# Kernel optimization log

Hardware: AMD Instinct MI355X
Metric: run time of the kernel (lower is better)

Reference implementation:

```python
import jax, jax.numpy as jnp
import numpy as np

N_NODES = 100000
D_FEAT = 128
N_ETYPES = 3
N_EDGES = 1000000


def setup_inputs() -> dict:
    key = jax.random.key(0)
    kx, ke = jax.random.split(key)
    x = jax.random.normal(kx, (N_NODES, D_FEAT), dtype=jnp.float32)
    # edges[t, 0] = src node ids, edges[t, 1] = dst node ids for edge type t
    edges = jax.random.randint(ke, (N_ETYPES, 2, N_EDGES), 0, N_NODES, dtype=jnp.int32)
    return {"x": x, "edges": edges}


def _copy_u_mean(x, src, dst, n_nodes):
    # gather source features and segment-mean them onto destination nodes;
    # nodes with zero in-degree get 0 (matching DGL copy_u + mean semantics)
    summed = jax.ops.segment_sum(x[src], dst, num_segments=n_nodes)  # [N, D]
    count = jax.ops.segment_sum(jnp.ones_like(dst, dtype=x.dtype), dst,
                                num_segments=n_nodes)  # [N]
    return jnp.where(count[:, None] > 0, summed / jnp.maximum(count, 1)[:, None],
                     jnp.zeros((), dtype=x.dtype))


def reference(x, edges):
    # sep=True: prepend the raw features before the per-edge-type aggregations
    parts = [x]
    for t in range(N_ETYPES):  # small fixed loop over structurally distinct edge types
        parts.append(_copy_u_mean(x, edges[t, 0], edges[t, 1], x.shape[0]))
    return jnp.concatenate(parts, axis=-1)  # [N, D*(1+N_ETYPES)]
```

## Files before the change

### kernel.cpp

```cpp
#include <hip/hip_runtime.h>
#include <hip/hip_bf16.h>

#define NN 100000
#define DF 128
#define NT 3
#define NE 1000000
#define DOUT 512
#define TOTH (NT * NN)
#define NBKT2 293
#define BCAP2 11264
#define CHUNK4 1024
#define CPT 245
#define CVT4_BLOCKS (NN * DF / 4 / 256)
#define EDGE4_BLOCKS ((NT * NE / 4 + 255) / 256)
#define SCAN_CHUNK 1024
#define NB1 ((TOTH + SCAN_CHUNK - 1) / SCAN_CHUNK)
#define NXCD 8
#define SLICE_BINS (TOTH / NXCD)

typedef __attribute__((ext_vector_type(4))) float f4v;
__device__ __forceinline__ void nts_f4(float4 v, float4* p) {
    f4v t; t.x = v.x; t.y = v.y; t.z = v.z; t.w = v.w;
    __builtin_nontemporal_store(t, (f4v*)p);
}

__global__ __launch_bounds__(256) void zero_k(int* __restrict__ p, int n) {
    int i = blockIdx.x * 256 + threadIdx.x;
    if (i < n) p[i] = 0;
}

__global__ __launch_bounds__(256) void cvtpart_k(const float4* __restrict__ x4,
                                                 uint2* __restrict__ xh2,
                                                 float4* __restrict__ out4,
                                                 const int4* __restrict__ edges4,
                                                 int* __restrict__ gcur,
                                                 int2* __restrict__ append) {
    __shared__ int cntB[512];
    __shared__ int startB[512];
    __shared__ int curB[512];
    __shared__ int targB[512];
    __shared__ int s[256];
    __shared__ int2 staged[4096];

    if (blockIdx.x < CVT4_BLOCKS) {
        int i = blockIdx.x * 256 + threadIdx.x;
        float4 v = x4[i];
        __hip_bfloat162 h0 = __float22bfloat162_rn(make_float2(v.x, v.y));
        __hip_bfloat162 h1 = __float22bfloat162_rn(make_float2(v.z, v.w));
        uint2 u; u.x = *(unsigned int*)&h0; u.y = *(unsigned int*)&h1;
        xh2[i] = u;
        int n = i >> 5;
        nts_f4(v, &out4[(size_t)n * (DOUT / 4) + (i & 31)]);
        return;
    }

    const int n4row = NE / 4;
    int b = blockIdx.x - CVT4_BLOCKS;
    int t = b / CPT;
    int c = b - t * CPT;
    int base4 = c * CHUNK4;
    int n4 = n4row - base4; if (n4 > CHUNK4) n4 = CHUNK4;
    int tid = threadIdx.x;
    for (int i = tid; i < 512; i += 256) { cntB[i] = 0; curB[i] = 0; }
    __syncthreads();

    int4 sv[4], dv[4];
    bool have[4];
#pragma unroll
    for (int j = 0; j < 4; j++) {
        int i4 = tid + j * 256;
        have[j] = (i4 < n4);
        if (have[j]) {
            sv[j] = edges4[(size_t)(2 * t) * n4row + base4 + i4];
            dv[j] = edges4[(size_t)(2 * t + 1) * n4row + base4 + i4];
            int b0 = t * NN;
            atomicAdd(&cntB[(b0 + dv[j].x) >> 10], 1);
            atomicAdd(&cntB[(b0 + dv[j].y) >> 10], 1);
            atomicAdd(&cntB[(b0 + dv[j].z) >> 10], 1);
            atomicAdd(&cntB[(b0 + dv[j].w) >> 10], 1);
        }
    }
    __syncthreads();
    int e0 = cntB[2 * tid], e1 = cntB[2 * tid + 1];
    int sum2 = e0 + e1;
    s[tid] = sum2;
    __syncthreads();
    for (int off = 1; off < 256; off <<= 1) {
        int tt = (tid >= off) ? s[tid - off] : 0;
        __syncthreads();
        s[tid] += tt;
        __syncthreads();
    }
    int run = s[tid] - sum2;
    startB[2 * tid] = run;
    startB[2 * tid + 1] = run + e0;
    __syncthreads();
#pragma unroll
    for (int j = 0; j < 4; j++) {
        if (have[j]) {
            int b0 = t * NN;
            int bin, bb, p;
            bin = b0 + dv[j].x; bb = bin >> 10; p = startB[bb] + atomicAdd(&curB[bb], 1); staged[p] = make_int2(sv[j].x, bin);
            bin = b0 + dv[j].y; bb = bin >> 10; p = startB[bb] + atomicAdd(&curB[bb], 1); staged[p] = make_int2(sv[j].y, bin);
            bin = b0 + dv[j].z; bb = bin >> 10; p = startB[bb] + atomicAdd(&curB[bb], 1); staged[p] = make_int2(sv[j].z, bin);
            bin = b0 + dv[j].w; bb = bin >> 10; p = startB[bb] + atomicAdd(&curB[bb], 1); staged[p] = make_int2(sv[j].w, bin);
        }
    }
    __syncthreads();
    for (int i = tid; i < NBKT2; i += 256)
        if (cntB[i] > 0) targB[i] = atomicAdd(&gcur[i], cntB[i]);
    __syncthreads();
    int total = n4 * 4;
    for (int i = tid; i < total; i += 256) {
        int2 e = staged[i];
        int bb = e.y >> 10;
        int gpos = targB[bb] + (i - startB[bb]);
        if (gpos < BCAP2) append[(size_t)bb * BCAP2 + gpos] = e;
    }
}

__global__ __launch_bounds__(512) void scanB_k(const int* __restrict__ gcur,
                                               int* __restrict__ bucketStart) {
    __shared__ int s[512];
    int tid = threadIdx.x;
    int v = 0;
    if (tid < NBKT2) { v = gcur[tid]; if (v > BCAP2) v = BCAP2; }
    s[tid] = v;
    __syncthreads();
    for (int off = 1; off < 512; off <<= 1) {
        int tt = (tid >= off) ? s[tid - off] : 0;
        __syncthreads();
        s[tid] += tt;
        __syncthreads();
    }
    if (tid < NBKT2) bucketStart[tid] = s[tid] - v;
}

__global__ __launch_bounds__(256) void binz_k(const int* __restrict__ gcur,
                                              const int* __restrict__ bucketStart,
                                              const int2* __restrict__ append,
                                              int* __restrict__ srcS,
                                              int2* __restrict__ cntoffs) {
    __shared__ int lcnt[1024], lofs[1024], lcur[1024];
    __shared__ int s[256];
    int bkt = blockIdx.x;
    int tid = threadIdx.x;
    int nb = gcur[bkt]; if (nb > BCAP2) nb = BCAP2;
    for (int i = tid; i < 1024; i += 256) { lcnt[i] = 0; lcur[i] = 0; }
    __syncthreads();
    const int2* ap = append + (size_t)bkt * BCAP2;
    for (int i = tid; i < nb; i += 256) atomicAdd(&lcnt[ap[i].y & 1023], 1);
    __syncthreads();
    int b4 = tid * 4;
    int v0 = lcnt[b4], v1 = lcnt[b4 + 1], v2 = lcnt[b4 + 2], v3 = lcnt[b4 + 3];
    int sum = v0 + v1 + v2 + v3;
    s[tid] = sum;
    __syncthreads();
    for (int off = 1; off < 256; off <<= 1) {
        int tt = (tid >= off) ? s[tid - off] : 0;
        __syncthreads();
        s[tid] += tt;
        __syncthreads();
    }
    int run = s[tid] - sum;
    lofs[b4] = run; run += v0;
    lofs[b4 + 1] = run; run += v1;
    lofs[b4 + 2] = run; run += v2;
    lofs[b4 + 3] = run;
    __syncthreads();
    int gbase = bucketStart[bkt];
    int binBase = bkt << 10;
    for (int i = tid; i < 1024 && binBase + i < TOTH; i += 256)
        cntoffs[binBase + i] = make_int2(lcnt[i], gbase + lofs[i]);
    for (int i = tid; i < nb; i += 256) {
        int2 e = ap[i];
        int lb = e.y & 1023;
        int pos = lofs[lb] + atomicAdd(&lcur[lb], 1);
        srcS[gbase + pos] = e.x;
    }
}

__global__ __launch_bounds__(256) void gather_agg_k(const uint2* __restrict__ xh2,
                                                    const int2* __restrict__ cntoffs,
                                                    const int* __restrict__ srcS,
                                                    float4* __restrict__ out4) {
    int gtid = blockIdx.x * 256 + threadIdx.x;
    int a = gtid >> 6;
    if (a >= TOTH) return;
    int lane = threadIdx.x & 63;
    int half = lane >> 5;
    int col = lane & 31;
    int t = a / NN;
    int n = a - t * NN;
    int2 co = cntoffs[a];
    int c = co.x;
    int base = co.y;
    float4 acc = make_float4(0.f, 0.f, 0.f, 0.f);
    int k = half;
    for (; k + 6 < c; k += 8) {
        int s0 = srcS[base + k];
        int s1 = srcS[base + k + 2];
        int s2 = srcS[base + k + 4];
        int s3 = srcS[base + k + 6];
        uint2 u0 = xh2[(size_t)s0 * 32 + col];
        uint2 u1 = xh2[(size_t)s1 * 32 + col];
        uint2 u2 = xh2[(size_t)s2 * 32 + col];
        uint2 u3 = xh2[(size_t)s3 * 32 + col];
        float2 p;
        p = __bfloat1622float2(*(__hip_bfloat162*)&u0.x); acc.x += p.x; acc.y += p.y;
        p = __bfloat1622float2(*(__hip_bfloat162*)&u0.y); acc.z += p.x; acc.w += p.y;
        p = __bfloat1622float2(*(__hip_bfloat162*)&u1.x); acc.x += p.x; acc.y += p.y;
        p = __bfloat1622float2(*(__hip_bfloat162*)&u1.y); acc.z += p.x; acc.w += p.y;
        p = __bfloat1622float2(*(__hip_bfloat162*)&u2.x); acc.x += p.x; acc.y += p.y;
        p = __bfloat1622float2(*(__hip_bfloat162*)&u2.y); acc.z += p.x; acc.w += p.y;
        p = __bfloat1622float2(*(__hip_bfloat162*)&u3.x); acc.x += p.x; acc.y += p.y;
        p = __bfloat1622float2(*(__hip_bfloat162*)&u3.y); acc.z += p.x; acc.w += p.y;
    }
    for (; k < c; k += 2) {
        int s0 = srcS[base + k];
        uint2 u0 = xh2[(size_t)s0 * 32 + col];
        float2 p;
        p = __bfloat1622float2(*(__hip_bfloat162*)&u0.x); acc.x += p.x; acc.y += p.y;
        p = __bfloat1622float2(*(__hip_bfloat162*)&u0.y); acc.z += p.x; acc.w += p.y;
    }
    acc.x += __shfl_xor(acc.x, 32, 64);
    acc.y += __shfl_xor(acc.y, 32, 64);
    acc.z += __shfl_xor(acc.z, 32, 64);
    acc.w += __shfl_xor(acc.w, 32, 64);
    if (half == 0) {
        float sc = (c > 0) ? 1.0f / (float)c : 0.0f;
        acc.x *= sc; acc.y *= sc; acc.z *= sc; acc.w *= sc;
        nts_f4(acc, &out4[(size_t)n * (DOUT / 4) + (DF / 4) + t * (DF / 4) + col]);
    }
}


__global__ __launch_bounds__(256) void hist_k(const int4* __restrict__ edges4,
                                              int* __restrict__ hist) {
    int i = blockIdx.x * 256 + threadIdx.x;
    if (i >= NT * NE / 4) return;
    int t = i / (NE / 4);
    int e4 = i - t * (NE / 4);
    int4 d = edges4[(size_t)(2 * t + 1) * (NE / 4) + e4];
    atomicAdd(&hist[t * NN + d.x], 1);
    atomicAdd(&hist[t * NN + d.y], 1);
    atomicAdd(&hist[t * NN + d.z], 1);
    atomicAdd(&hist[t * NN + d.w], 1);
}

__global__ __launch_bounds__(256) void scan1_k(const int* __restrict__ hist,
                                               int* __restrict__ offs,
                                               int* __restrict__ bsum) {
    __shared__ int s[256];
    int tid = threadIdx.x;
    int base = blockIdx.x * SCAN_CHUNK + tid * 4;
    int v0 = 0, v1 = 0, v2 = 0, v3 = 0;
    if (base + 0 < TOTH) v0 = hist[base + 0];
    if (base + 1 < TOTH) v1 = hist[base + 1];
    if (base + 2 < TOTH) v2 = hist[base + 2];
    if (base + 3 < TOTH) v3 = hist[base + 3];
    int sum = v0 + v1 + v2 + v3;
    s[tid] = sum;
    __syncthreads();
    for (int off = 1; off < 256; off <<= 1) {
        int t = (tid >= off) ? s[tid - off] : 0;
        __syncthreads();
        s[tid] += t;
        __syncthreads();
    }
    int run = s[tid] - sum;
    if (tid == 255) bsum[blockIdx.x] = s[255];
    if (base + 0 < TOTH) { offs[base + 0] = run; run += v0; }
    if (base + 1 < TOTH) { offs[base + 1] = run; run += v1; }
    if (base + 2 < TOTH) { offs[base + 2] = run; run += v2; }
    if (base + 3 < TOTH) { offs[base + 3] = run; run += v3; }
}

__global__ __launch_bounds__(512) void scan2_k(int* __restrict__ bsum) {
    __shared__ int s[512];
    int tid = threadIdx.x;
    int v = (tid < NB1) ? bsum[tid] : 0;
    s[tid] = v;
    __syncthreads();
    for (int off = 1; off < 512; off <<= 1) {
        int t = (tid >= off) ? s[tid - off] : 0;
        __syncthreads();
        s[tid] += t;
        __syncthreads();
    }
    if (tid < NB1) bsum[tid] = s[tid] - v;
}

__global__ __launch_bounds__(256) void scan3_k(int* __restrict__ offs,
                                               const int* __restrict__ bsum) {
    int i = blockIdx.x * 256 + threadIdx.x;
    if (i < TOTH) offs[i] += bsum[i / SCAN_CHUNK];
}

__global__ __launch_bounds__(256) void fill_csr_k(const int4* __restrict__ edges4,
                                                  int* __restrict__ offs,
                                                  int* __restrict__ srcS) {
    int slice = blockIdx.x & (NXCD - 1);
    int i = (blockIdx.x >> 3) * 256 + threadIdx.x;
    if (i >= NT * NE / 4) return;
    int t = i / (NE / 4);
    int e4 = i - t * (NE / 4);
    int4 sv = edges4[(size_t)(2 * t) * (NE / 4) + e4];
    int4 dv = edges4[(size_t)(2 * t + 1) * (NE / 4) + e4];
    int b0 = t * NN;
    int bin;
    bin = b0 + dv.x; if (bin / SLICE_BINS == slice) srcS[atomicAdd(&offs[bin], 1)] = sv.x;
    bin = b0 + dv.y; if (bin / SLICE_BINS == slice) srcS[atomicAdd(&offs[bin], 1)] = sv.y;
    bin = b0 + dv.z; if (bin / SLICE_BINS == slice) srcS[atomicAdd(&offs[bin], 1)] = sv.z;
    bin = b0 + dv.w; if (bin / SLICE_BINS == slice) srcS[atomicAdd(&offs[bin], 1)] = sv.w;
}

__global__ __launch_bounds__(256) void gather_f32_k(const float4* __restrict__ x4,
                                                    const int* __restrict__ cnt,
                                                    const int* __restrict__ offs,
                                                    const int* __restrict__ srcS,
                                                    float4* __restrict__ out4) {
    int gtid = blockIdx.x * 256 + threadIdx.x;
    int w = gtid >> 6;
    int lane = threadIdx.x & 63;
    int half = lane >> 5;
    int col = lane & 31;
    if (w < NN / 2) {
        int n = 2 * w + half;
        out4[(size_t)n * (DOUT / 4) + col] = x4[(size_t)n * (DF / 4) + col];
        return;
    }
    int a = w - NN / 2;
    if (a >= TOTH) return;
    int t = a / NN;
    int n = a - t * NN;
    int c = cnt[a];
    int base = offs[a] - c;
    float4 acc = make_float4(0.f, 0.f, 0.f, 0.f);
    for (int k = half; k < c; k += 2) {
        int s0 = srcS[base + k];
        float4 v0 = x4[(size_t)s0 * (DF / 4) + col];
        acc.x += v0.x; acc.y += v0.y; acc.z += v0.z; acc.w += v0.w;
    }
    acc.x += __shfl_xor(acc.x, 32, 64);
    acc.y += __shfl_xor(acc.y, 32, 64);
    acc.z += __shfl_xor(acc.z, 32, 64);
    acc.w += __shfl_xor(acc.w, 32, 64);
    if (half == 0) {
        float sc = (c > 0) ? 1.0f / (float)c : 0.0f;
        acc.x *= sc; acc.y *= sc; acc.z *= sc; acc.w *= sc;
        out4[(size_t)n * (DOUT / 4) + (DF / 4) + t * (DF / 4) + col] = acc;
    }
}

extern "C" void kernel_launch(void* const* d_in, const int* in_sizes, int n_in,
                              void* d_out, int out_size, void* d_ws, size_t ws_size,
                              hipStream_t stream) {
    const float* x = (const float*)d_in[0];
    const int* edges = (const int*)d_in[1];
    float4* out4 = (float4*)d_out;

    const int covBlocks = (TOTH + 255) / 256;
    const int aggBlocks = (TOTH * 64 + 255) / 256;

    size_t appendInts = (size_t)NBKT2 * BCAP2 * 2;
    size_t fastInts = 1024 + appendInts + 2 * (size_t)TOTH +
                      (size_t)NN * DF / 2 + (size_t)NT * NE + 64;
    if (ws_size >= fastInts * 4) {
        int* gcur = (int*)d_ws;
        int* bucketStart = gcur + 512;
        int2* append = (int2*)(bucketStart + 512);
        int2* cntoffs = (int2*)((int*)d_ws + 1024 + appendInts);
        unsigned int* xh = (unsigned int*)(cntoffs + TOTH);
        int* srcS = (int*)(xh + (size_t)NN * DF / 2);

        hipLaunchKernelGGL(zero_k, dim3(2), dim3(256), 0, stream, gcur, 512);
        hipLaunchKernelGGL(cvtpart_k, dim3(CVT4_BLOCKS + NT * CPT), dim3(256), 0,
                           stream, (const float4*)x, (uint2*)xh, (float4*)d_out,
                           (const int4*)edges, gcur, append);
        hipLaunchKernelGGL(scanB_k, dim3(1), dim3(512), 0, stream, gcur, bucketStart);
        hipLaunchKernelGGL(binz_k, dim3(NBKT2), dim3(256), 0, stream,
                           gcur, bucketStart, append, srcS, cntoffs);
        hipLaunchKernelGGL(gather_agg_k, dim3(aggBlocks), dim3(256), 0, stream,
                           (const uint2*)xh, cntoffs, srcS, out4);
        return;
    }

    int* hist = (int*)d_ws;
    int* offs = hist + TOTH;
    int* bsum = offs + TOTH;
    int* srcS = bsum + 1024;
    const int nWaves = NN / 2 + TOTH;
    const int gatherBlocks = (nWaves + 3) / 4;
    hipLaunchKernelGGL(zero_k, dim3(covBlocks), dim3(256), 0, stream, hist, TOTH);
    hipLaunchKernelGGL(hist_k, dim3(EDGE4_BLOCKS), dim3(256), 0, stream,
                       (const int4*)edges, hist);
    hipLaunchKernelGGL(scan1_k, dim3(NB1), dim3(256), 0, stream, hist, offs, bsum);
    hipLaunchKernelGGL(scan2_k, dim3(1), dim3(512), 0, stream, bsum);
    hipLaunchKernelGGL(scan3_k, dim3(covBlocks), dim3(256), 0, stream, offs, bsum);
    hipLaunchKernelGGL(fill_csr_k, dim3(EDGE4_BLOCKS * NXCD), dim3(256), 0, stream,
                       (const int4*)edges, offs, srcS);
    hipLaunchKernelGGL(gather_f32_k, dim3(gatherBlocks), dim3(256), 0, stream,
                       (const float4*)x, hist, offs, srcS, out4);
}
```

Baseline: 218.6 us.

## Fold bucket scan into binz kernel, reorder partition blocks first, widen binz

Removes the separate single-block scanB kernel launch: each binz block now redundantly computes the 293-bucket prefix sum in shared memory to get its global base. binz blocks grow from 256 to 1024 threads so each handles one bin per thread and strides the bucket edges by 1024. The fused convert/partition kernel now schedules partition blocks ahead of conversion blocks, so the slower edge-partition work starts first. The costs are redundant scan work per block and more synchronisation in larger blocks.

Measured after the change: 211.1 us. 3.4% less time.

```diff
diff --git a/kernel.cpp b/kernel.cpp
--- a/kernel.cpp
+++ b/kernel.cpp
@@ -11,6 +11,7 @@
 #define BCAP2 11264
 #define CHUNK4 1024
 #define CPT 245
+#define PART_BLOCKS (NT * CPT)
 #define CVT4_BLOCKS (NN * DF / 4 / 256)
 #define EDGE4_BLOCKS ((NT * NE / 4 + 255) / 256)
 #define SCAN_CHUNK 1024
@@ -42,8 +43,8 @@
     __shared__ int s[256];
     __shared__ int2 staged[4096];
 
-    if (blockIdx.x < CVT4_BLOCKS) {
-        int i = blockIdx.x * 256 + threadIdx.x;
+    if (blockIdx.x >= PART_BLOCKS) {
+        int i = (blockIdx.x - PART_BLOCKS) * 256 + threadIdx.x;
         float4 v = x4[i];
         __hip_bfloat162 h0 = __float22bfloat162_rn(make_float2(v.x, v.y));
         __hip_bfloat162 h1 = __float22bfloat162_rn(make_float2(v.z, v.w));
@@ -55,7 +56,7 @@
     }
 
     const int n4row = NE / 4;
-    int b = blockIdx.x - CVT4_BLOCKS;
+    int b = blockIdx.x;
     int t = b / CPT;
     int c = b - t * CPT;
     int base4 = c * CHUNK4;
@@ -119,60 +120,62 @@
     }
 }
 
-__global__ __launch_bounds__(512) void scanB_k(const int* __restrict__ gcur,
-                                               int* __restrict__ bucketStart) {
-    __shared__ int s[512];
-    int tid = threadIdx.x;
-    int v = 0;
-    if (tid < NBKT2) { v = gcur[tid]; if (v > BCAP2) v = BCAP2; }
-    s[tid] = v;
-    __syncthreads();
-    for (int off = 1; off < 512; off <<= 1) {
-        int tt = (tid >= off) ? s[tid - off] : 0;
-        __syncthreads();
-        s[tid] += tt;
-        __syncthreads();
-    }
-    if (tid < NBKT2) bucketStart[tid] = s[tid] - v;
-}
-
-__global__ __launch_bounds__(256) void binz_k(const int* __restrict__ gcur,
-                                              const int* __restrict__ bucketStart,
-                                              const int2* __restrict__ append,
-                                              int* __restrict__ srcS,
-                                              int2* __restrict__ cntoffs) {
+__global__ __launch_bounds__(1024) void binz_k(const int* __restrict__ gcur,
+                                               const int2* __restrict__ append,
+                                               int* __restrict__ srcS,
+                                               int2* __restrict__ cntoffs) {
     __shared__ int lcnt[1024], lofs[1024], lcur[1024];
     __shared__ int s[256];
+    __shared__ int sB[512];
     int bkt = blockIdx.x;
     int tid = threadIdx.x;
-    int nb = gcur[bkt]; if (nb > BCAP2) nb = BCAP2;
-    for (int i = tid; i < 1024; i += 256) { lcnt[i] = 0; lcur[i] = 0; }
-    __syncthreads();
+    int nbRaw = gcur[bkt];
+    int nb = nbRaw < BCAP2 ? nbRaw : BCAP2;
+    if (tid < 512) {
+        int v = 0;
+        if (tid < NBKT2) { v = gcur[tid]; if (v > BCAP2) v = BCAP2; }
+        sB[tid] = v;
+    }
+    lcnt[tid] = 0; lcur[tid] = 0;
+    __syncthreads();
+    for (int off = 1; off < 512; off <<= 1) {
+        int tt = 0;
+        if (tid < 512 && tid >= off) tt = sB[tid - off];
+        __syncthreads();
+        if (tid < 512) sB[tid] += tt;
+        __syncthreads();
+    }
+    int gbase = (bkt == 0) ? 0 : sB[bkt - 1];
     const int2* ap = append + (size_t)bkt * BCAP2;
-    for (int i = tid; i < nb; i += 256) atomicAdd(&lcnt[ap[i].y & 1023], 1);
+    for (int i = tid; i < nb; i += 1024) atomicAdd(&lcnt[ap[i].y & 1023], 1);
     __syncthreads();
     int b4 = tid * 4;
-    int v0 = lcnt[b4], v1 = lcnt[b4 + 1], v2 = lcnt[b4 + 2], v3 = lcnt[b4 + 3];
-    int sum = v0 + v1 + v2 + v3;
-    s[tid] = sum;
+    int v0 = 0, v1 = 0, v2 = 0, v3 = 0, sum = 0;
+    if (tid < 256) {
+        v0 = lcnt[b4]; v1 = lcnt[b4 + 1]; v2 = lcnt[b4 + 2]; v3 = lcnt[b4 + 3];
+        sum = v0 + v1 + v2 + v3;
+        s[tid] = sum;
+    }
     __syncthreads();
     for (int off = 1; off < 256; off <<= 1) {
-        int tt = (tid >= off) ? s[tid - off] : 0;
-        __syncthreads();
-        s[tid] += tt;
-        __syncthreads();
-    }
-    int run = s[tid] - sum;
-    lofs[b4] = run; run += v0;
-    lofs[b4 + 1] = run; run += v1;
-    lofs[b4 + 2] = run; run += v2;
-    lofs[b4 + 3] = run;
-    __syncthreads();
-    int gbase = bucketStart[bkt];
+        int tt = 0;
+        if (tid < 256 && tid >= off) tt = s[tid - off];
+        __syncthreads();
+        if (tid < 256) s[tid] += tt;
+        __syncthreads();
+    }
+    if (tid < 256) {
+        int run = s[tid] - sum;
+        lofs[b4] = run; run += v0;
+        lofs[b4 + 1] = run; run += v1;
+        lofs[b4 + 2] = run; run += v2;
+        lofs[b4 + 3] = run;
+    }
+    __syncthreads();
     int binBase = bkt << 10;
-    for (int i = tid; i < 1024 && binBase + i < TOTH; i += 256)
-        cntoffs[binBase + i] = make_int2(lcnt[i], gbase + lofs[i]);
-    for (int i = tid; i < nb; i += 256) {
+    if (binBase + tid < TOTH)
+        cntoffs[binBase + tid] = make_int2(lcnt[tid], gbase + lofs[tid]);
+    for (int i = tid; i < nb; i += 1024) {
         int2 e = ap[i];
         int lb = e.y & 1023;
         int pos = lofs[lb] + atomicAdd(&lcur[lb], 1);
@@ -368,19 +371,17 @@
                       (size_t)NN * DF / 2 + (size_t)NT * NE + 64;
     if (ws_size >= fastInts * 4) {
         int* gcur = (int*)d_ws;
-        int* bucketStart = gcur + 512;
-        int2* append = (int2*)(bucketStart + 512);
+        int2* append = (int2*)(gcur + 1024);
         int2* cntoffs = (int2*)((int*)d_ws + 1024 + appendInts);
         unsigned int* xh = (unsigned int*)(cntoffs + TOTH);
         int* srcS = (int*)(xh + (size_t)NN * DF / 2);
 
         hipLaunchKernelGGL(zero_k, dim3(2), dim3(256), 0, stream, gcur, 512);
-        hipLaunchKernelGGL(cvtpart_k, dim3(CVT4_BLOCKS + NT * CPT), dim3(256), 0,
+        hipLaunchKernelGGL(cvtpart_k, dim3(PART_BLOCKS + CVT4_BLOCKS), dim3(256), 0,
                            stream, (const float4*)x, (uint2*)xh, (float4*)d_out,
                            (const int4*)edges, gcur, append);
-        hipLaunchKernelGGL(scanB_k, dim3(1), dim3(512), 0, stream, gcur, bucketStart);
-        hipLaunchKernelGGL(binz_k, dim3(NBKT2), dim3(256), 0, stream,
-                           gcur, bucketStart, append, srcS, cntoffs);
+        hipLaunchKernelGGL(binz_k, dim3(NBKT2), dim3(1024), 0, stream,
+                           gcur, append, srcS, cntoffs);
         hipLaunchKernelGGL(gather_agg_k, dim3(aggBlocks), dim3(256), 0, stream,
                            (const uint2*)xh, cntoffs, srcS, out4);
         return;
```
